# Kernel tuning notes

Measured on AMD Instinct MI355X. Metric: run time of the kernel, lower is better.

## Reference

```python
import jax, jax.numpy as jnp
import numpy as np

B, N, C, D = 16, 1024, 768, 384

def setup_inputs() -> dict:
    key = jax.random.key(0)
    ks = jax.random.split(key, 12)
    s_in = 1.0 / np.sqrt(C)
    s_d = 1.0 / np.sqrt(D)
    return {
        "x": jax.random.normal(ks[0], (B, N, C), dtype=jnp.float32),
        "adj": jax.random.uniform(ks[1], (B, N, N), dtype=jnp.float32),
        "W_theta": jax.random.uniform(ks[2], (C, D), minval=-s_in, maxval=s_in),
        "b_theta": jax.random.uniform(ks[3], (D,), minval=-s_in, maxval=s_in),
        "W_phi": jax.random.uniform(ks[4], (C, D), minval=-s_in, maxval=s_in),
        "b_phi": jax.random.uniform(ks[5], (D,), minval=-s_in, maxval=s_in),
        "W_g": jax.random.uniform(ks[6], (C, D), minval=-s_in, maxval=s_in),
        "b_g": jax.random.uniform(ks[7], (D,), minval=-s_in, maxval=s_in),
        "W_out": jax.random.uniform(ks[8], (D, C), minval=-s_d, maxval=s_d),
        "b_out": jax.random.uniform(ks[9], (C,), minval=-s_d, maxval=s_d),
    }

def reference(x, adj, W_theta, b_theta, W_phi, b_phi, W_g, b_g, W_out, b_out):
    # projections: [B,N,C] @ [C,D] -> [B,N,D]
    theta = x @ W_theta + b_theta
    phi = x @ W_phi + b_phi
    g = x @ W_g + b_g
    # unscaled attention scores with multiplicative adjacency mask
    attn = jnp.einsum('bnd,bmd->bnm', theta, phi) * adj  # [B,N,N]
    attn = jax.nn.softmax(attn, axis=-1)  # dropout is identity in eval mode
    out = jnp.einsum('bnm,bmd->bnd', attn, g)  # [B,N,D]
    out = out @ W_out + b_out  # [B,N,C]
    return out + x
```

## Files before the change

kernel.cpp:

```cpp
#include <hip/hip_runtime.h>
#include <hip/hip_bf16.h>

typedef __hip_bfloat16 bf16;
typedef short bf16x8 __attribute__((ext_vector_type(8)));
typedef float f32x4 __attribute__((ext_vector_type(4)));

constexpr int Bb = 16, Nn = 1024, Cc = 768, Dd = 384;

static __device__ __forceinline__ f32x4 mfma16(bf16x8 a, bf16x8 b, f32x4 c) {
    return __builtin_amdgcn_mfma_f32_16x16x32_bf16(a, b, c, 0, 0, 0);
}
static __device__ __forceinline__ short f2b(float v) {
    __hip_bfloat16 h = __float2bfloat16(v);
    return *reinterpret_cast<short*>(&h);
}
static __device__ __forceinline__ unsigned pack2(float lo, float hi) {
    return ((unsigned)(unsigned short)f2b(hi) << 16) | (unsigned short)(unsigned)f2b(lo);
}
static __device__ __forceinline__ float b2f(bf16 x) { return __bfloat162float(x); }

__global__ __launch_bounds__(256) void cast_bf16(
    const float* __restrict__ in, uint4* __restrict__ out)
{
    const size_t i = (size_t)blockIdx.x * 256 + threadIdx.x;
    const float4 a = reinterpret_cast<const float4*>(in)[i * 2];
    const float4 b = reinterpret_cast<const float4*>(in)[i * 2 + 1];
    uint4 v;
    v.x = pack2(a.x, a.y);
    v.y = pack2(a.z, a.w);
    v.z = pack2(b.x, b.y);
    v.w = pack2(b.z, b.w);
    out[i] = v;
}

__global__ __launch_bounds__(256) void pack_bias(
    const float* __restrict__ bt, const float* __restrict__ bp,
    const float* __restrict__ bg, float* __restrict__ out)
{
    const int i = blockIdx.x * 256 + threadIdx.x;
    if (i < 384) out[i] = bt[i];
    else if (i < 768) out[i] = bp[i - 384];
    else if (i < 1152) out[i] = bg[i - 768];
}

__global__ __launch_bounds__(256) void transpose_cast(
    const float* __restrict__ in, bf16* __restrict__ out, int K, int N)
{
    __shared__ float t[32][33];
    const int n0 = blockIdx.x * 32, k0 = blockIdx.y * 32;
    const int tx = threadIdx.x & 31, ty = threadIdx.x >> 5;
#pragma unroll
    for (int i = 0; i < 4; i++)
        t[ty + i * 8][tx] = in[(size_t)(k0 + ty + i * 8) * N + n0 + tx];
    __syncthreads();
#pragma unroll
    for (int i = 0; i < 4; i++)
        out[(size_t)(n0 + ty + i * 8) * K + k0 + tx] = __float2bfloat16(t[tx][ty + i * 8]);
}

template <typename TA, int EPI>
__global__ __launch_bounds__(256) void gemm_mfma(
    const TA* __restrict__ A, const bf16* __restrict__ BT,
    const float* __restrict__ bias, const float* __restrict__ resid,
    void* __restrict__ outp, int K, int Nout)
{
    __shared__ short As[128 * 40];
    __shared__ short Bs[128 * 40];
    const int tid = threadIdx.x;
    const int lane = tid & 63, w = tid >> 6;
    const int quad = lane >> 4, c = lane & 15;
    const int row0 = blockIdx.x * 128, col0 = blockIdx.y * 128;
    const int wm = (w & 1) * 64, wn = (w >> 1) * 64;

    const f32x4 fz = {0.f, 0.f, 0.f, 0.f};
    f32x4 acc[4][4];
#pragma unroll
    for (int i = 0; i < 4; i++)
#pragma unroll
        for (int j = 0; j < 4; j++) acc[i][j] = fz;

    for (int k0 = 0; k0 < K; k0 += 32) {
        __syncthreads();
        if (sizeof(TA) == 4) {
            const float* Af = (const float*)A;
#pragma unroll
            for (int u = 0; u < 4; u++) {
                const int id = u * 256 + tid;
                const int r = id >> 3, c4 = (id & 7) * 4;
                const float4 v = *reinterpret_cast<const float4*>(Af + (size_t)(row0 + r) * K + k0 + c4);
                uint2 p;
                p.x = pack2(v.x, v.y);
                p.y = pack2(v.z, v.w);
                *reinterpret_cast<uint2*>(&As[r * 40 + c4]) = p;
            }
        } else {
            const bf16* Ab = (const bf16*)A;
#pragma unroll
            for (int u = 0; u < 2; u++) {
                const int id = u * 256 + tid;
                const int r = id >> 2, c8 = (id & 3) * 8;
                const uint4 v = *reinterpret_cast<const uint4*>(Ab + (size_t)(row0 + r) * K + k0 + c8);
                *reinterpret_cast<uint4*>(&As[r * 40 + c8]) = v;
            }
        }
#pragma unroll
        for (int u = 0; u < 2; u++) {
            const int id = u * 256 + tid;
            const int r = id >> 2, c8 = (id & 3) * 8;
            const uint4 v = *reinterpret_cast<const uint4*>(BT + (size_t)(col0 + r) * K + k0 + c8);
            *reinterpret_cast<uint4*>(&Bs[r * 40 + c8]) = v;
        }
        __syncthreads();

        bf16x8 af[4], bfr[4];
#pragma unroll
        for (int i = 0; i < 4; i++)
            af[i] = *reinterpret_cast<const bf16x8*>(&As[(wm + i * 16 + c) * 40 + quad * 8]);
#pragma unroll
        for (int j = 0; j < 4; j++)
            bfr[j] = *reinterpret_cast<const bf16x8*>(&Bs[(wn + j * 16 + c) * 40 + quad * 8]);
#pragma unroll
        for (int i = 0; i < 4; i++)
#pragma unroll
            for (int j = 0; j < 4; j++)
                acc[i][j] = mfma16(af[i], bfr[j], acc[i][j]);
    }

    const size_t SZc = (size_t)Bb * Nn * Dd;
#pragma unroll
    for (int i = 0; i < 4; i++) {
        const int rowb = row0 + wm + i * 16 + quad * 4;
#pragma unroll
        for (int j = 0; j < 4; j++) {
            const int col = col0 + wn + j * 16 + c;
            const float bcol = bias[col];
#pragma unroll
            for (int r = 0; r < 4; r++) {
                float v = acc[i][j][r] + bcol;
                const int rr = rowb + r;
                if (EPI == 0) {
                    ((bf16*)outp)[(size_t)rr * Nout + col] = __float2bfloat16(v);
                } else if (EPI == 1) {
                    const int bb = rr >> 10, m = rr & 1023;
                    ((bf16*)outp)[((size_t)(bb * Nout + col)) * 1024 + m] = __float2bfloat16(v);
                } else if (EPI == 2) {
                    v += resid[(size_t)rr * Nout + col];
                    ((float*)outp)[(size_t)rr * Nout + col] = v;
                } else {
                    const int seg = col / 384;
                    const int cl = col - seg * 384;
                    bf16* base = (bf16*)outp;
                    if (seg < 2) {
                        base[(size_t)seg * SZc + (size_t)rr * Dd + cl] = __float2bfloat16(v);
                    } else {
                        const int bb = rr >> 10, m = rr & 1023;
                        base[2 * SZc + ((size_t)(bb * Dd + cl)) * 1024 + m] = __float2bfloat16(v);
                    }
                }
            }
        }
    }
}

__global__ __launch_bounds__(256, 1) void flash_attn(
    const bf16* __restrict__ theta, const bf16* __restrict__ phi,
    const bf16* __restrict__ gT, const float* __restrict__ adj,
    bf16* __restrict__ O)
{
    __shared__ short phs[2][32 * 392];
    __shared__ short gts[2][384 * 40];
    __shared__ short pls[4][16 * 40];

    const int tid = threadIdx.x;
    const int lane = tid & 63, w = tid >> 6;
    const int quad = lane >> 4, c = lane & 15;
    const int qb = blockIdx.x, b = blockIdx.y;

    const size_t thbase = ((size_t)b * Nn + qb * 64 + w * 16 + c) * Dd;
    bf16x8 ath[12];
#pragma unroll
    for (int dq = 0; dq < 12; dq++)
        ath[dq] = *reinterpret_cast<const bf16x8*>(theta + thbase + dq * 32 + quad * 8);

    const bf16* phibase = phi + (size_t)b * Nn * Dd;
    const bf16* gtb = gT + (size_t)b * Dd * Nn;
    const float* arow = adj + ((size_t)b * Nn + qb * 64 + w * 16 + quad * 4) * Nn;

    uint4 vph[6], vgt[6];
    float av0[4], av1[4];

    auto prefetch = [&](int n0) {
#pragma unroll
        for (int u = 0; u < 6; u++) {
            const int id = u * 256 + tid;
            vph[u] = *reinterpret_cast<const uint4*>(
                phibase + (size_t)(n0 + id / 48) * Dd + (id % 48) * 8);
        }
#pragma unroll
        for (int u = 0; u < 6; u++) {
            const int id = u * 256 + tid;
            vgt[u] = *reinterpret_cast<const uint4*>(
                gtb + (size_t)(id >> 2) * Nn + n0 + (id & 3) * 8);
        }
#pragma unroll
        for (int r = 0; r < 4; r++) {
            av0[r] = arow[(size_t)r * Nn + n0 + c];
            av1[r] = arow[(size_t)r * Nn + n0 + 16 + c];
        }
    };

    const f32x4 fz = {0.f, 0.f, 0.f, 0.f};
    f32x4 o[24];
#pragma unroll
    for (int t = 0; t < 24; t++) o[t] = fz;
    float mrow[4], lrow[4];
#pragma unroll
    for (int r = 0; r < 4; r++) { mrow[r] = -INFINITY; lrow[r] = 0.f; }

    prefetch(0);

    for (int it = 0; it < 32; ++it) {
        const int n0 = it * 32;
        short* ph = (short*)phs[it & 1];
        short* gt = (short*)gts[it & 1];

#pragma unroll
        for (int u = 0; u < 6; u++) {
            const int id = u * 256 + tid;
            *reinterpret_cast<uint4*>(&ph[(id / 48) * 392 + (id % 48) * 8]) = vph[u];
        }
#pragma unroll
        for (int u = 0; u < 6; u++) {
            const int id = u * 256 + tid;
            *reinterpret_cast<uint4*>(&gt[(id >> 2) * 40 + (id & 3) * 8]) = vgt[u];
        }
        float a0[4], a1[4];
#pragma unroll
        for (int r = 0; r < 4; r++) { a0[r] = av0[r]; a1[r] = av1[r]; }

        if (it < 31) prefetch(n0 + 32);

        __syncthreads();

        f32x4 s0 = fz, s1 = fz;
#pragma unroll
        for (int dq = 0; dq < 12; dq++) {
            const bf16x8 b0 = *reinterpret_cast<const bf16x8*>(&ph[c * 392 + dq * 32 + quad * 8]);
            const bf16x8 b1 = *reinterpret_cast<const bf16x8*>(&ph[(16 + c) * 392 + dq * 32 + quad * 8]);
            s0 = mfma16(ath[dq], b0, s0);
            s1 = mfma16(ath[dq], b1, s1);
        }

        float p0[4], p1[4], alpha[4];
#pragma unroll
        for (int r = 0; r < 4; r++) {
            const float v0 = s0[r] * a0[r];
            const float v1 = s1[r] * a1[r];
            float t = fmaxf(v0, v1);
#pragma unroll
            for (int msk = 1; msk < 16; msk <<= 1) t = fmaxf(t, __shfl_xor(t, msk));
            const float mn = fmaxf(mrow[r], t);
            alpha[r] = __expf(mrow[r] - mn);
            mrow[r] = mn;
            p0[r] = __expf(v0 - mn);
            p1[r] = __expf(v1 - mn);
            float u = p0[r] + p1[r];
#pragma unroll
            for (int msk = 1; msk < 16; msk <<= 1) u += __shfl_xor(u, msk);
            lrow[r] = lrow[r] * alpha[r] + u;
        }
#pragma unroll
        for (int t = 0; t < 24; t++)
#pragma unroll
            for (int r = 0; r < 4; r++) o[t][r] *= alpha[r];

        short* pl = (short*)pls[w];
#pragma unroll
        for (int r = 0; r < 4; r++) {
            pl[(quad * 4 + r) * 40 + c] = f2b(p0[r]);
            pl[(quad * 4 + r) * 40 + 16 + c] = f2b(p1[r]);
        }
        const bf16x8 ap = *reinterpret_cast<const bf16x8*>(&pl[c * 40 + quad * 8]);
#pragma unroll
        for (int dn = 0; dn < 24; dn++) {
            const bf16x8 bg = *reinterpret_cast<const bf16x8*>(&gt[(dn * 16 + c) * 40 + quad * 8]);
            o[dn] = mfma16(ap, bg, o[dn]);
        }
    }

    float inv[4];
#pragma unroll
    for (int r = 0; r < 4; r++) inv[r] = 1.0f / lrow[r];
    bf16* orow = O + ((size_t)b * Nn + qb * 64 + w * 16 + quad * 4) * Dd;
#pragma unroll
    for (int dn = 0; dn < 24; dn++)
#pragma unroll
        for (int r = 0; r < 4; r++)
            orow[(size_t)r * Dd + dn * 16 + c] = __float2bfloat16(o[dn][r] * inv[r]);
}

__global__ __launch_bounds__(256) void proj_gemm(
    const float* __restrict__ A, const float* __restrict__ W,
    const float* __restrict__ bias, bf16* __restrict__ out,
    int M, int K, int Nd)
{
    __shared__ float Asm[16][65];
    __shared__ float Bsm[16][65];
    const int tid = threadIdx.x;
    const int tx = tid & 15, ty = tid >> 4;
    const int row0 = blockIdx.x * 64, col0 = blockIdx.y * 64;
    float acc[4][4] = {};
    for (int k0 = 0; k0 < K; k0 += 16) {
        {
            const int m = tid >> 2, kq = (tid & 3) * 4;
            const float* p = A + (size_t)(row0 + m) * K + k0 + kq;
#pragma unroll
            for (int j = 0; j < 4; j++) Asm[kq + j][m] = p[j];
        }
        {
            const int k = tid >> 4, n4 = (tid & 15) * 4;
            const float* p = W + (size_t)(k0 + k) * Nd + col0 + n4;
#pragma unroll
            for (int j = 0; j < 4; j++) Bsm[k][n4 + j] = p[j];
        }
        __syncthreads();
#pragma unroll
        for (int k = 0; k < 16; k++) {
            float a[4], bv[4];
#pragma unroll
            for (int j = 0; j < 4; j++) a[j] = Asm[k][ty * 4 + j];
#pragma unroll
            for (int j = 0; j < 4; j++) bv[j] = Bsm[k][tx * 4 + j];
#pragma unroll
            for (int i = 0; i < 4; i++)
#pragma unroll
                for (int j = 0; j < 4; j++) acc[i][j] += a[i] * bv[j];
        }
        __syncthreads();
    }
#pragma unroll
    for (int i = 0; i < 4; i++) {
        const int row = row0 + ty * 4 + i;
#pragma unroll
        for (int j = 0; j < 4; j++) {
            const int col = col0 + tx * 4 + j;
            out[(size_t)row * Nd + col] = __float2bfloat16(acc[i][j] + bias[col]);
        }
    }
}

__global__ __launch_bounds__(256) void fused_attn(
    const float* __restrict__ x, const float* __restrict__ adj,
    const float* __restrict__ W_theta, const float* __restrict__ b_theta,
    const bf16* __restrict__ phi, const bf16* __restrict__ g,
    const float* __restrict__ W_out, const float* __restrict__ b_out,
    float* __restrict__ out)
{
    __shared__ float xs[Cc];
    __shared__ float th[Dd];
    __shared__ float s[Nn];
    __shared__ float Os[Dd];
    __shared__ float red[256];
    const int tid = threadIdx.x;
    const int n = blockIdx.x, b = blockIdx.y;
    const int lane = tid & 63, wave = tid >> 6;
    const size_t row = (size_t)b * Nn + n;
    const size_t baseD = (size_t)b * Nn * Dd;
    for (int c = tid; c < Cc; c += 256) xs[c] = x[row * Cc + c];
    __syncthreads();
    for (int d = tid; d < Dd; d += 256) {
        float acc = b_theta[d];
#pragma unroll 8
        for (int c = 0; c < Cc; c++) acc += xs[c] * W_theta[(size_t)c * Dd + d];
        th[d] = acc;
    }
    __syncthreads();
    for (int m = wave; m < Nn; m += 4) {
        const bf16* prow = phi + baseD + (size_t)m * Dd;
        float partial = 0.f;
#pragma unroll
        for (int j = 0; j < 6; j++) {
            const int d = lane + 64 * j;
            partial += th[d] * b2f(prow[d]);
        }
#pragma unroll
        for (int off = 32; off > 0; off >>= 1) partial += __shfl_down(partial, off);
        if (lane == 0)
            s[m] = partial * adj[(size_t)b * Nn * Nn + (size_t)n * Nn + m];
    }
    __syncthreads();
    float mx = -1e30f;
    for (int i = tid; i < Nn; i += 256) mx = fmaxf(mx, s[i]);
    red[tid] = mx; __syncthreads();
    for (int st = 128; st > 0; st >>= 1) {
        if (tid < st) red[tid] = fmaxf(red[tid], red[tid + st]);
        __syncthreads();
    }
    mx = red[0]; __syncthreads();
    float lsum = 0.f;
    for (int i = tid; i < Nn; i += 256) {
        const float e = __expf(s[i] - mx);
        s[i] = e;
        lsum += e;
    }
    red[tid] = lsum; __syncthreads();
    for (int st = 128; st > 0; st >>= 1) {
        if (tid < st) red[tid] += red[tid + st];
        __syncthreads();
    }
    const float inv = 1.0f / red[0];
    __syncthreads();
    for (int d = tid; d < Dd; d += 256) {
        float acc = 0.f;
#pragma unroll 8
        for (int m = 0; m < Nn; m++) acc += s[m] * b2f(g[baseD + (size_t)m * Dd + d]);
        Os[d] = acc * inv;
    }
    __syncthreads();
    for (int c = tid; c < Cc; c += 256) {
        float acc = b_out[c] + xs[c];
#pragma unroll 8
        for (int d = 0; d < Dd; d++) acc += Os[d] * W_out[(size_t)d * Cc + c];
        out[row * Cc + c] = acc;
    }
}

extern "C" void kernel_launch(void* const* d_in, const int* in_sizes, int n_in,
                              void* d_out, int out_size, void* d_ws, size_t ws_size,
                              hipStream_t stream)
{
    const float* x       = (const float*)d_in[0];
    const float* adj     = (const float*)d_in[1];
    const float* W_theta = (const float*)d_in[2];
    const float* b_theta = (const float*)d_in[3];
    const float* W_phi   = (const float*)d_in[4];
    const float* b_phi   = (const float*)d_in[5];
    const float* W_g     = (const float*)d_in[6];
    const float* b_g     = (const float*)d_in[7];
    const float* W_out   = (const float*)d_in[8];
    const float* b_out   = (const float*)d_in[9];
    float* out = (float*)d_out;

    const int M = Bb * Nn;
    const size_t SZ  = (size_t)Bb * Nn * Dd;
    const size_t SZX = (size_t)M * Cc;
    const size_t WSZ = (size_t)Cc * Dd;
    const size_t NEED_OLD = (4 * WSZ + 4 * SZ) * sizeof(bf16);
    const size_t NEED_NEW = (4 * WSZ + 4 * SZ + SZX) * sizeof(bf16)
                          + 1152 * sizeof(float);

    dim3 blk(256);

    if (ws_size >= NEED_NEW) {
        bf16* WtT   = (bf16*)d_ws;
        bf16* WpT   = WtT + WSZ;
        bf16* WgT   = WpT + WSZ;
        bf16* WoT   = WgT + WSZ;
        bf16* theta = WoT + WSZ;
        bf16* phi   = theta + SZ;
        bf16* gT    = phi + SZ;
        bf16* O     = gT + SZ;
        bf16* xb    = O + SZ;
        float* biasP = (float*)(xb + SZX);

        cast_bf16<<<dim3((unsigned)(SZX / 2048)), blk, 0, stream>>>(x, (uint4*)xb);
        transpose_cast<<<dim3(Dd / 32, Cc / 32), blk, 0, stream>>>(W_theta, WtT, Cc, Dd);
        transpose_cast<<<dim3(Dd / 32, Cc / 32), blk, 0, stream>>>(W_phi,   WpT, Cc, Dd);
        transpose_cast<<<dim3(Dd / 32, Cc / 32), blk, 0, stream>>>(W_g,     WgT, Cc, Dd);
        transpose_cast<<<dim3(Cc / 32, Dd / 32), blk, 0, stream>>>(W_out,   WoT, Dd, Cc);
        pack_bias<<<dim3(5), blk, 0, stream>>>(b_theta, b_phi, b_g, biasP);

        gemm_mfma<bf16, 3><<<dim3(M / 128, 1152 / 128), blk, 0, stream>>>(
            xb, WtT, biasP, nullptr, theta, Cc, 1152);

        flash_attn<<<dim3(Nn / 64, Bb), blk, 0, stream>>>(theta, phi, gT, adj, O);

        gemm_mfma<bf16, 2><<<dim3(M / 128, Cc / 128), blk, 0, stream>>>(
            O, WoT, b_out, x, out, Dd, Cc);
    } else if (ws_size >= NEED_OLD) {
        bf16* WtT   = (bf16*)d_ws;
        bf16* WpT   = WtT + WSZ;
        bf16* WgT   = WpT + WSZ;
        bf16* WoT   = WgT + WSZ;
        bf16* theta = WoT + WSZ;
        bf16* phi   = theta + SZ;
        bf16* gT    = phi + SZ;
        bf16* O     = gT + SZ;

        transpose_cast<<<dim3(Dd / 32, Cc / 32), blk, 0, stream>>>(W_theta, WtT, Cc, Dd);
        transpose_cast<<<dim3(Dd / 32, Cc / 32), blk, 0, stream>>>(W_phi,   WpT, Cc, Dd);
        transpose_cast<<<dim3(Dd / 32, Cc / 32), blk, 0, stream>>>(W_g,     WgT, Cc, Dd);
        transpose_cast<<<dim3(Cc / 32, Dd / 32), blk, 0, stream>>>(W_out,   WoT, Dd, Cc);

        dim3 gp(M / 128, Dd / 128);
        gemm_mfma<float, 0><<<gp, blk, 0, stream>>>(x, WtT, b_theta, nullptr, theta, Cc, Dd);
        gemm_mfma<float, 0><<<gp, blk, 0, stream>>>(x, WpT, b_phi,   nullptr, phi,   Cc, Dd);
        gemm_mfma<float, 1><<<gp, blk, 0, stream>>>(x, WgT, b_g,     nullptr, gT,    Cc, Dd);

        flash_attn<<<dim3(Nn / 64, Bb), blk, 0, stream>>>(theta, phi, gT, adj, O);

        dim3 go(M / 128, Cc / 128);
        gemm_mfma<bf16, 2><<<go, blk, 0, stream>>>(O, WoT, b_out, x, out, Dd, Cc);
    } else {
        bf16* phi = (bf16*)d_ws;
        bf16* g   = phi + SZ;
        dim3 gproj(M / 64, Dd / 64);
        proj_gemm<<<gproj, blk, 0, stream>>>(x, W_phi, b_phi, phi, M, Cc, Dd);
        proj_gemm<<<gproj, blk, 0, stream>>>(x, W_g, b_g, g, M, Cc, Dd);
        fused_attn<<<dim3(Nn, Bb), blk, 0, stream>>>(
            x, adj, W_theta, b_theta, phi, g, W_out, b_out, out);
    }
}
```

Before: 391.7 us.

## Split flash attention over key range and merge partial softmax results

Splits the flash-attention key dimension into two halves launched as a third grid dimension, writing unnormalized fp32 partial outputs plus row max and sum to workspace. A new combine kernel rescales and merges the halves into the bf16 output. The register double-buffered prefetch and the double-buffered shared memory are removed and launch bounds are relaxed to two blocks per CU. The aim is more blocks in flight and better occupancy, since the original grid had only 256 blocks. The cost is extra fp32 partial traffic, an extra kernel launch, and loads that are no longer overlapped with compute.

```diff
diff --git a/kernel.cpp b/kernel.cpp
--- a/kernel.cpp
+++ b/kernel.cpp
@@ -162,19 +162,23 @@
     }
 }
 
-__global__ __launch_bounds__(256, 1) void flash_attn(
+template <int SPLIT>
+__global__ __launch_bounds__(256, 2) void flash_attn(
     const bf16* __restrict__ theta, const bf16* __restrict__ phi,
     const bf16* __restrict__ gT, const float* __restrict__ adj,
-    bf16* __restrict__ O)
-{
-    __shared__ short phs[2][32 * 392];
-    __shared__ short gts[2][384 * 40];
+    bf16* __restrict__ O, float* __restrict__ Sp, float* __restrict__ ml)
+{
+    __shared__ short phs[32 * 392];
+    __shared__ short gts[384 * 40];
     __shared__ short pls[4][16 * 40];
 
     const int tid = threadIdx.x;
     const int lane = tid & 63, w = tid >> 6;
     const int quad = lane >> 4, c = lane & 15;
     const int qb = blockIdx.x, b = blockIdx.y;
+    const int sp = SPLIT ? blockIdx.z : 0;
+    const int n_lo = SPLIT ? sp * (Nn / 2) : 0;
+    const int n_hi = SPLIT ? n_lo + Nn / 2 : Nn;
 
     const size_t thbase = ((size_t)b * Nn + qb * 64 + w * 16 + c) * Dd;
     bf16x8 ath[12];
@@ -182,33 +186,6 @@
     for (int dq = 0; dq < 12; dq++)
         ath[dq] = *reinterpret_cast<const bf16x8*>(theta + thbase + dq * 32 + quad * 8);
 
-    const bf16* phibase = phi + (size_t)b * Nn * Dd;
-    const bf16* gtb = gT + (size_t)b * Dd * Nn;
-    const float* arow = adj + ((size_t)b * Nn + qb * 64 + w * 16 + quad * 4) * Nn;
-
-    uint4 vph[6], vgt[6];
-    float av0[4], av1[4];
-
-    auto prefetch = [&](int n0) {
-#pragma unroll
-        for (int u = 0; u < 6; u++) {
-            const int id = u * 256 + tid;
-            vph[u] = *reinterpret_cast<const uint4*>(
-                phibase + (size_t)(n0 + id / 48) * Dd + (id % 48) * 8);
-        }
-#pragma unroll
-        for (int u = 0; u < 6; u++) {
-            const int id = u * 256 + tid;
-            vgt[u] = *reinterpret_cast<const uint4*>(
-                gtb + (size_t)(id >> 2) * Nn + n0 + (id & 3) * 8);
-        }
-#pragma unroll
-        for (int r = 0; r < 4; r++) {
-            av0[r] = arow[(size_t)r * Nn + n0 + c];
-            av1[r] = arow[(size_t)r * Nn + n0 + 16 + c];
-        }
-    };
-
     const f32x4 fz = {0.f, 0.f, 0.f, 0.f};
     f32x4 o[24];
 #pragma unroll
@@ -217,45 +194,45 @@
 #pragma unroll
     for (int r = 0; r < 4; r++) { mrow[r] = -INFINITY; lrow[r] = 0.f; }
 
-    prefetch(0);
-
-    for (int it = 0; it < 32; ++it) {
-        const int n0 = it * 32;
-        short* ph = (short*)phs[it & 1];
-        short* gt = (short*)gts[it & 1];
-
-#pragma unroll
-        for (int u = 0; u < 6; u++) {
-            const int id = u * 256 + tid;
-            *reinterpret_cast<uint4*>(&ph[(id / 48) * 392 + (id % 48) * 8]) = vph[u];
-        }
-#pragma unroll
-        for (int u = 0; u < 6; u++) {
-            const int id = u * 256 + tid;
-            *reinterpret_cast<uint4*>(&gt[(id >> 2) * 40 + (id & 3) * 8]) = vgt[u];
-        }
-        float a0[4], a1[4];
-#pragma unroll
-        for (int r = 0; r < 4; r++) { a0[r] = av0[r]; a1[r] = av1[r]; }
-
-        if (it < 31) prefetch(n0 + 32);
-
+    for (int n0 = n_lo; n0 < n_hi; n0 += 32) {
+        __syncthreads();
+        {
+            const bf16* src = phi + ((size_t)b * Nn + n0) * Dd;
+#pragma unroll
+            for (int u = 0; u < 6; u++) {
+                const int id = u * 256 + tid;
+                const int r = id / 48, cc = (id % 48) * 8;
+                const uint4 v = *reinterpret_cast<const uint4*>(src + (size_t)r * Dd + cc);
+                *reinterpret_cast<uint4*>(&phs[r * 392 + cc]) = v;
+            }
+        }
+        {
+            const bf16* src = gT + ((size_t)b * Dd) * Nn + n0;
+#pragma unroll
+            for (int u = 0; u < 6; u++) {
+                const int id = u * 256 + tid;
+                const int r = id >> 2, cc = (id & 3) * 8;
+                const uint4 v = *reinterpret_cast<const uint4*>(src + (size_t)r * Nn + cc);
+                *reinterpret_cast<uint4*>(&gts[r * 40 + cc]) = v;
+            }
+        }
         __syncthreads();
 
         f32x4 s0 = fz, s1 = fz;
 #pragma unroll
         for (int dq = 0; dq < 12; dq++) {
-            const bf16x8 b0 = *reinterpret_cast<const bf16x8*>(&ph[c * 392 + dq * 32 + quad * 8]);
-            const bf16x8 b1 = *reinterpret_cast<const bf16x8*>(&ph[(16 + c) * 392 + dq * 32 + quad * 8]);
+            const bf16x8 b0 = *reinterpret_cast<const bf16x8*>(&phs[c * 392 + dq * 32 + quad * 8]);
+            const bf16x8 b1 = *reinterpret_cast<const bf16x8*>(&phs[(16 + c) * 392 + dq * 32 + quad * 8]);
             s0 = mfma16(ath[dq], b0, s0);
             s1 = mfma16(ath[dq], b1, s1);
         }
 
+        const float* arow = adj + ((size_t)b * Nn + qb * 64 + w * 16 + quad * 4) * Nn + n0;
         float p0[4], p1[4], alpha[4];
 #pragma unroll
         for (int r = 0; r < 4; r++) {
-            const float v0 = s0[r] * a0[r];
-            const float v1 = s1[r] * a1[r];
+            const float v0 = s0[r] * arow[(size_t)r * Nn + c];
+            const float v1 = s1[r] * arow[(size_t)r * Nn + 16 + c];
             float t = fmaxf(v0, v1);
 #pragma unroll
             for (int msk = 1; msk < 16; msk <<= 1) t = fmaxf(t, __shfl_xor(t, msk));
@@ -280,23 +257,63 @@
             pl[(quad * 4 + r) * 40 + c] = f2b(p0[r]);
             pl[(quad * 4 + r) * 40 + 16 + c] = f2b(p1[r]);
         }
+        __syncthreads();
         const bf16x8 ap = *reinterpret_cast<const bf16x8*>(&pl[c * 40 + quad * 8]);
 #pragma unroll
         for (int dn = 0; dn < 24; dn++) {
-            const bf16x8 bg = *reinterpret_cast<const bf16x8*>(&gt[(dn * 16 + c) * 40 + quad * 8]);
+            const bf16x8 bg = *reinterpret_cast<const bf16x8*>(&gts[(dn * 16 + c) * 40 + quad * 8]);
             o[dn] = mfma16(ap, bg, o[dn]);
         }
     }
 
-    float inv[4];
-#pragma unroll
-    for (int r = 0; r < 4; r++) inv[r] = 1.0f / lrow[r];
-    bf16* orow = O + ((size_t)b * Nn + qb * 64 + w * 16 + quad * 4) * Dd;
-#pragma unroll
-    for (int dn = 0; dn < 24; dn++)
-#pragma unroll
-        for (int r = 0; r < 4; r++)
-            orow[(size_t)r * Dd + dn * 16 + c] = __float2bfloat16(o[dn][r] * inv[r]);
+    const int rowb = qb * 64 + w * 16 + quad * 4;
+    if (SPLIT) {
+        float* srow = Sp + ((size_t)sp * Bb * Nn + (size_t)b * Nn + rowb) * Dd;
+#pragma unroll
+        for (int dn = 0; dn < 24; dn++)
+#pragma unroll
+            for (int r = 0; r < 4; r++)
+                srow[(size_t)r * Dd + dn * 16 + c] = o[dn][r];
+        if (c == 0) {
+#pragma unroll
+            for (int r = 0; r < 4; r++) {
+                const size_t rid = (size_t)sp * Bb * Nn + (size_t)b * Nn + rowb + r;
+                ml[rid * 2]     = mrow[r];
+                ml[rid * 2 + 1] = lrow[r];
+            }
+        }
+    } else {
+        float inv[4];
+#pragma unroll
+        for (int r = 0; r < 4; r++) inv[r] = 1.0f / lrow[r];
+        bf16* orow = O + ((size_t)b * Nn + rowb) * Dd;
+#pragma unroll
+        for (int dn = 0; dn < 24; dn++)
+#pragma unroll
+            for (int r = 0; r < 4; r++)
+                orow[(size_t)r * Dd + dn * 16 + c] = __float2bfloat16(o[dn][r] * inv[r]);
+    }
+}
+
+__global__ __launch_bounds__(256) void attn_combine(
+    const float* __restrict__ Sp, const float* __restrict__ ml,
+    bf16* __restrict__ O)
+{
+    constexpr size_t M = (size_t)Bb * Nn;
+    const size_t idx = (size_t)blockIdx.x * 256 + threadIdx.x;
+    const size_t e0 = idx * 4;
+    const size_t row = e0 / Dd;
+    const float m1 = ml[row * 2],           l1 = ml[row * 2 + 1];
+    const float m2 = ml[(M + row) * 2],     l2 = ml[(M + row) * 2 + 1];
+    const float mx = fmaxf(m1, m2);
+    const float w1 = __expf(m1 - mx), w2 = __expf(m2 - mx);
+    const float inv = 1.0f / (w1 * l1 + w2 * l2);
+    const float4 a = *reinterpret_cast<const float4*>(Sp + e0);
+    const float4 b = *reinterpret_cast<const float4*>(Sp + M * Dd + e0);
+    uint2 p;
+    p.x = pack2((w1 * a.x + w2 * b.x) * inv, (w1 * a.y + w2 * b.y) * inv);
+    p.y = pack2((w1 * a.z + w2 * b.z) * inv, (w1 * a.w + w2 * b.w) * inv);
+    *reinterpret_cast<uint2*>(O + e0) = p;
 }
 
 __global__ __launch_bounds__(256) void proj_gemm(
@@ -448,6 +465,8 @@
     const size_t NEED_OLD = (4 * WSZ + 4 * SZ) * sizeof(bf16);
     const size_t NEED_NEW = (4 * WSZ + 4 * SZ + SZX) * sizeof(bf16)
                           + 1152 * sizeof(float);
+    const size_t NEED_SPLIT = NEED_NEW
+                          + (2 * SZ + 4 * (size_t)M) * sizeof(float);
 
     dim3 blk(256);
 
@@ -462,6 +481,8 @@
         bf16* O     = gT + SZ;
         bf16* xb    = O + SZ;
         float* biasP = (float*)(xb + SZX);
+        float* Sp    = biasP + 1152;
+        float* mlp   = Sp + 2 * SZ;
 
         cast_bf16<<<dim3((unsigned)(SZX / 2048)), blk, 0, stream>>>(x, (uint4*)xb);
         transpose_cast<<<dim3(Dd / 32, Cc / 32), blk, 0, stream>>>(W_theta, WtT, Cc, Dd);
@@ -473,7 +494,14 @@
         gemm_mfma<bf16, 3><<<dim3(M / 128, 1152 / 128), blk, 0, stream>>>(
             xb, WtT, biasP, nullptr, theta, Cc, 1152);
 
-        flash_attn<<<dim3(Nn / 64, Bb), blk, 0, stream>>>(theta, phi, gT, adj, O);
+        if (ws_size >= NEED_SPLIT) {
+            flash_attn<1><<<dim3(Nn / 64, Bb, 2), blk, 0, stream>>>(
+                theta, phi, gT, adj, nullptr, Sp, mlp);
+            attn_combine<<<dim3((unsigned)(SZ / 1024)), blk, 0, stream>>>(Sp, mlp, O);
+        } else {
+            flash_attn<0><<<dim3(Nn / 64, Bb, 1), blk, 0, stream>>>(
+                theta, phi, gT, adj, O, nullptr, nullptr);
+        }
 
         gemm_mfma<bf16, 2><<<dim3(M / 128, Cc / 128), blk, 0, stream>>>(
             O, WoT, b_out, x, out, Dd, Cc);
@@ -497,7 +525,8 @@
         gemm_mfma<float, 0><<<gp, blk, 0, stream>>>(x, WpT, b_phi,   nullptr, phi,   Cc, Dd);
         gemm_mfma<float, 1><<<gp, blk, 0, stream>>>(x, WgT, b_g,     nullptr, gT,    Cc, Dd);
 
-        flash_attn<<<dim3(Nn / 64, Bb), blk, 0, stream>>>(theta, phi, gT, adj, O);
+        flash_attn<0><<<dim3(Nn / 64, Bb, 1), blk, 0, stream>>>(
+            theta, phi, gT, adj, O, nullptr, nullptr);
 
         dim3 go(M / 128, Cc / 128);
         gemm_mfma<bf16, 2><<<go, blk, 0, stream>>>(O, WoT, b_out, x, out, Dd, Cc);
```

Result: faster. 341.8 us (-12.7%).
